# Kernel optimization log

Measured on AMD Instinct MI355X. Metric: run time of the kernel, lower is better.

Reference implementation:

```python
import jax, jax.numpy as jnp
import numpy as np

B, S, D = 1, 4096, 1024
H = 16
HD = D // H  # 64
ROPE_THETA = 10000.0
NEG_INF = -1e9


def setup_inputs() -> dict:
    key = jax.random.key(0)
    ks = jax.random.split(key, 6)
    x = jax.random.normal(ks[0], (B, S, D), dtype=jnp.float32)
    # rotary frequencies: freqs_cis = exp(i * t * theta^{-2j/hd}), j in [0, hd/2)
    inv_freq = 1.0 / (ROPE_THETA ** (jnp.arange(0, HD, 2, dtype=jnp.float32) / HD))  # [HD/2]
    angles = jnp.arange(S, dtype=jnp.float32)[:, None] * inv_freq[None, :]  # [S, HD/2]
    freqs_cos = jnp.cos(angles)
    freqs_sin = jnp.sin(angles)
    # causal additive mask [S, S]
    mask = jnp.where(jnp.triu(jnp.ones((S, S), dtype=bool), k=1), NEG_INF, 0.0).astype(jnp.float32)
    scale = 0.02
    wq = jax.random.normal(ks[1], (D, D), dtype=jnp.float32) * scale
    wk = jax.random.normal(ks[2], (D, D), dtype=jnp.float32) * scale
    wv = jax.random.normal(ks[3], (D, D), dtype=jnp.float32) * scale
    wo = jax.random.normal(ks[4], (D, D), dtype=jnp.float32) * scale
    return {"x": x, "freqs_cos": freqs_cos, "freqs_sin": freqs_sin, "mask": mask,
            "wq": wq, "wk": wk, "wv": wv, "wo": wo}


def _apply_rope(t, cos, sin):
    # t: [B, S, H, HD]; cos/sin: [S, HD/2] -> broadcast [1, S, 1, HD/2]
    tr = t.reshape(*t.shape[:-1], HD // 2, 2)
    te, to = tr[..., 0], tr[..., 1]
    c = cos[None, :, None, :]
    s = sin[None, :, None, :]
    # complex multiply (te + i*to) * (c + i*s)
    oe = te * c - to * s
    oo = te * s + to * c
    return jnp.stack([oe, oo], axis=-1).reshape(t.shape)


def reference(x, freqs_cos, freqs_sin, mask, wq, wk, wv, wo):
    b, s, d = x.shape
    q = (x @ wq.T).reshape(b, s, H, HD)
    k = (x @ wk.T).reshape(b, s, H, HD)
    v = (x @ wv.T).reshape(b, s, H, HD)
    q = _apply_rope(q, freqs_cos, freqs_sin)
    k = _apply_rope(k, freqs_cos, freqs_sin)
    # [B, H, S, HD]
    q = q.transpose(0, 2, 1, 3)
    k = k.transpose(0, 2, 1, 3)
    v = v.transpose(0, 2, 1, 3)
    scores = jnp.einsum('bhqd,bhkd->bhqk', q, k) / jnp.sqrt(jnp.float32(HD))
    scores = scores + mask[None, None, :, :]
    probs = jax.nn.softmax(scores.astype(jnp.float32), axis=-1).astype(q.dtype)
    out = jnp.einsum('bhqk,bhkd->bhqd', probs, v)
    out = out.transpose(0, 2, 1, 3).reshape(b, s, d)
    return out @ wo.T
```

## Files before the change

### kernel.cpp

```cpp
#include <hip/hip_runtime.h>
#include <stdint.h>

typedef _Float16 f16;
typedef _Float16 v2h __attribute__((ext_vector_type(2)));
typedef _Float16 v4h __attribute__((ext_vector_type(4)));
typedef _Float16 v8h __attribute__((ext_vector_type(8)));
typedef float    v4f __attribute__((ext_vector_type(4)));

#define SEQ 4096
#define NH  16
#define DM  1024
#define QSCALE 0.18033688011112042f
#define MBASE 8.0f

__device__ __forceinline__ float exp2_(float x) {
#if __has_builtin(__builtin_amdgcn_exp2f)
  return __builtin_amdgcn_exp2f(x);
#else
  return exp2f(x);
#endif
}

__device__ __forceinline__ void gload_lds16(const void* g, void* l) {
  __builtin_amdgcn_global_load_lds((const __attribute__((address_space(1))) void*)g,
                                   (__attribute__((address_space(3))) void*)l,
                                   16, 0, 0);
}

#define NX 4194304
#define NW 1048576
__global__ void convert_kernel(const float* __restrict__ x,
                               const float* __restrict__ wq, const float* __restrict__ wk,
                               const float* __restrict__ wv, const float* __restrict__ wo,
                               f16* __restrict__ xf, f16* __restrict__ W, f16* __restrict__ Wo) {
  size_t e = ((size_t)blockIdx.x * 256 + threadIdx.x) * 4;
  const float* src; f16* dst;
  if (e < (size_t)NX) { src = x + e; dst = xf + e; }
  else {
    size_t j = e - NX; int wi = (int)(j >> 20); size_t off = j & (NW - 1);
    src = (wi == 0 ? wq : wi == 1 ? wk : wi == 2 ? wv : wo) + off;
    dst = (wi < 3 ? W + (size_t)wi * NW : Wo) + off;
  }
  v4f v = *(const v4f*)src;
  v4h o = { (f16)v.x, (f16)v.y, (f16)v.z, (f16)v.w };
  *(v4h*)dst = o;
}

template <typename OUTT>
__global__ __launch_bounds__(256, 2) void gemm_bt_f16(const f16* __restrict__ A,
                                                      const f16* __restrict__ B,
                                                      OUTT* __restrict__ C,
                                                      int M, int N, int K) {
  __shared__ __align__(16) f16 As[128 * 64];
  __shared__ __align__(16) f16 Bs[128 * 64];
  const int t = threadIdx.x;
  const int w = t >> 6, l = t & 63, quad = l >> 4, l15 = l & 15;
  const int wm = w & 1, wn = w >> 1;
  const int m0 = blockIdx.y * 128, n0 = blockIdx.x * 128;

  v4f acc[4][4];
#pragma unroll
  for (int i = 0; i < 4; ++i)
#pragma unroll
    for (int j = 0; j < 4; ++j) acc[i][j] = v4f{0.f, 0.f, 0.f, 0.f};

  const int nkt = K >> 6;
  for (int kt = 0; kt < nkt; ++kt) {
    __syncthreads();
#pragma unroll
    for (int i = 0; i < 4; ++i) {
      int c = i * 256 + t; int r = c >> 3, cc = c & 7; int sc = cc ^ (r & 7);
      gload_lds16(A + (size_t)(m0 + r) * K + kt * 64 + sc * 8, As + c * 8);
      gload_lds16(B + (size_t)(n0 + r) * K + kt * 64 + sc * 8, Bs + c * 8);
    }
    __syncthreads();
#pragma unroll
    for (int ks = 0; ks < 2; ++ks) {
      v8h af[4], bf[4];
#pragma unroll
      for (int i = 0; i < 4; ++i) {
        int ra = wm * 64 + i * 16 + l15;
        af[i] = *(const v8h*)(As + ra * 64 + (((ks * 4 + quad) ^ (ra & 7)) * 8));
        int rb = wn * 64 + i * 16 + l15;
        bf[i] = *(const v8h*)(Bs + rb * 64 + (((ks * 4 + quad) ^ (rb & 7)) * 8));
      }
#pragma unroll
      for (int i = 0; i < 4; ++i)
#pragma unroll
        for (int j = 0; j < 4; ++j)
          acc[i][j] = __builtin_amdgcn_mfma_f32_16x16x32_f16(af[i], bf[j], acc[i][j], 0, 0, 0);
    }
  }
#pragma unroll
  for (int i = 0; i < 4; ++i) {
    int m = m0 + wm * 64 + i * 16 + quad * 4;
#pragma unroll
    for (int j = 0; j < 4; ++j) {
      int n = n0 + wn * 64 + j * 16 + l15;
#pragma unroll
      for (int rg = 0; rg < 4; ++rg)
        C[(size_t)(m + rg) * N + n] = (OUTT)acc[i][j][rg];
    }
  }
}

__global__ void rope_kernel(const f16* __restrict__ qkv, const float* __restrict__ fc,
                            const float* __restrict__ fs, f16* __restrict__ Qh,
                            f16* __restrict__ Kh) {
  int idx = blockIdx.x * 256 + threadIdx.x;
  int s = idx >> 9, r = idx & 511, h = r >> 5, i = r & 31;
  size_t base = (size_t)s * 3072 + h * 64 + 2 * i;
  float qe = (float)qkv[base], qo = (float)qkv[base + 1];
  float ke = (float)qkv[base + 1024], ko = (float)qkv[base + 1025];
  float c = fc[s * 32 + i], sn = fs[s * 32 + i];
  size_t ob = ((size_t)(h * 4096 + s)) * 64 + 2 * i;
  v2h qo2 = { (f16)((qe * c - qo * sn) * QSCALE), (f16)((qe * sn + qo * c) * QSCALE) };
  v2h ko2 = { (f16)(ke * c - ko * sn), (f16)(ke * sn + ko * c) };
  *(v2h*)(Qh + ob) = qo2;
  *(v2h*)(Kh + ob) = ko2;
}

__global__ void vtrans_kernel(const f16* __restrict__ qkv, f16* __restrict__ Vt) {
  __shared__ __align__(16) f16 T[64][72];
  int h = blockIdx.x >> 6, sb = blockIdx.x & 63;
  int t = threadIdx.x, s0 = sb * 64;
#pragma unroll
  for (int i = 0; i < 2; ++i) {
    int r = i * 32 + (t >> 3), c8 = t & 7;
    *(v8h*)(&T[r][c8 * 8]) = *(const v8h*)(qkv + (size_t)(s0 + r) * 3072 + 2048 + h * 64 + c8 * 8);
  }
  __syncthreads();
#pragma unroll
  for (int i = 0; i < 4; ++i) {
    int idx = i * 256 + t;
    int d = idx >> 4;
    int sq = (idx & 15) * 4;
    int g = sq >> 5;
    int s32 = sq & 31;
    int kap = ((s32 >> 2) & 3) * 8 + (s32 >> 4) * 4;
    v4h o = { T[sq + 0][d], T[sq + 1][d], T[sq + 2][d], T[sq + 3][d] };
    *(v4h*)(Vt + (size_t)(h * 64 + d) * 4096 + s0 + g * 32 + kap) = o;
  }
}

__global__ __launch_bounds__(256, 2) void flash_kernel(const f16* __restrict__ Qh,
                                                       const f16* __restrict__ Kh,
                                                       const f16* __restrict__ Vt,
                                                       f16* __restrict__ attn) {
  __shared__ __align__(16) f16 SM[16384];
  f16* Ks = SM;
  f16* Vs = SM + 8192;
  int u = blockIdx.x >> 4, h = blockIdx.x & 15;
  int qb = (u < 16) ? (31 - u) : (u - 16);
  int t = threadIdx.x, w = t >> 6, l = t & 63, quad = l >> 4, l15 = l & 15;
  int q0w = qb * 128 + w * 32;

  v8h qf[2][2];
#pragma unroll
  for (int qt = 0; qt < 2; ++qt)
#pragma unroll
    for (int ks = 0; ks < 2; ++ks)
      qf[qt][ks] = *(const v8h*)(Qh + ((size_t)(h * 4096 + q0w + qt * 16 + l15)) * 64 + ks * 32 + quad * 8);

  v4f av[2][4];
#pragma unroll
  for (int qt = 0; qt < 2; ++qt)
#pragma unroll
    for (int db = 0; db < 4; ++db) av[qt][db] = v4f{0.f, 0.f, 0.f, 0.f};
  float lrun[2] = { 0.f, 0.f };

  const int kbhi = 2 * qb + 1;
  const int c0 = t, c1 = 256 + t;
  const int r0 = c0 >> 3, sc0 = (c0 & 7) ^ (r0 & 7);
  const int r1 = c1 >> 3, sc1 = (c1 & 7) ^ (r1 & 7);
  const f16* KhB = Kh + (size_t)h * 4096 * 64;
  const f16* VtB = Vt + (size_t)h * 64 * 4096;

  gload_lds16(KhB + (size_t)r0 * 64 + sc0 * 8, Ks + c0 * 8);
  gload_lds16(KhB + (size_t)r1 * 64 + sc1 * 8, Ks + c1 * 8);
  gload_lds16(VtB + (size_t)r0 * 4096 + sc0 * 8, Vs + c0 * 8);
  gload_lds16(VtB + (size_t)r1 * 4096 + sc1 * 8, Vs + c1 * 8);

  for (int kb = 0; kb <= kbhi; ++kb) {
    __syncthreads();
    if (kb < kbhi) {
      int nb = (kb + 1) & 1;
      int koff = (kb + 1) * 64;
      gload_lds16(KhB + (size_t)(koff + r0) * 64 + sc0 * 8, Ks + nb * 4096 + c0 * 8);
      gload_lds16(KhB + (size_t)(koff + r1) * 64 + sc1 * 8, Ks + nb * 4096 + c1 * 8);
      gload_lds16(VtB + (size_t)r0 * 4096 + koff + sc0 * 8, Vs + nb * 4096 + c0 * 8);
      gload_lds16(VtB + (size_t)r1 * 4096 + koff + sc1 * 8, Vs + nb * 4096 + c1 * 8);
    }
    if (kb * 64 > q0w + 31) continue;
    const f16* Kc = Ks + (kb & 1) * 4096;
    const f16* Vc = Vs + (kb & 1) * 4096;

    v8h kf[4][2];
#pragma unroll
    for (int kt = 0; kt < 4; ++kt)
#pragma unroll
      for (int ks = 0; ks < 2; ++ks) {
        int r = kt * 16 + l15;
        kf[kt][ks] = *(const v8h*)(Kc + r * 64 + (((ks * 4 + quad) ^ (r & 7)) * 8));
      }

#pragma unroll
    for (int qt = 0; qt < 2; ++qt) {
      int qtb = q0w + qt * 16;
      if (kb * 64 > qtb + 15) continue;
      v4f st[4];
#pragma unroll
      for (int kt = 0; kt < 4; ++kt) {
        v4f z = v4f{ -MBASE, -MBASE, -MBASE, -MBASE };
        z = __builtin_amdgcn_mfma_f32_16x16x32_f16(kf[kt][0], qf[qt][0], z, 0, 0, 0);
        st[kt] = __builtin_amdgcn_mfma_f32_16x16x32_f16(kf[kt][1], qf[qt][1], z, 0, 0, 0);
      }
      if (kb * 64 + 63 > qtb) {
        int qg = qtb + l15;
#pragma unroll
        for (int kt = 0; kt < 4; ++kt)
#pragma unroll
          for (int jj = 0; jj < 4; ++jj) {
            int kg = kb * 64 + kt * 16 + quad * 4 + jj;
            if (kg > qg) st[kt][jj] = -1e30f;
          }
      }
      v4h pf[4];
      float rs = 0.f;
#pragma unroll
      for (int kt = 0; kt < 4; ++kt)
#pragma unroll
        for (int jj = 0; jj < 4; ++jj) {
          float p = exp2_(st[kt][jj]);
          rs += p;
          pf[kt][jj] = (f16)p;
        }
      lrun[qt] += rs;
      v8h pg[2];
#pragma unroll
      for (int g = 0; g < 2; ++g) {
        pg[g][0] = pf[2 * g][0]; pg[g][1] = pf[2 * g][1];
        pg[g][2] = pf[2 * g][2]; pg[g][3] = pf[2 * g][3];
        pg[g][4] = pf[2 * g + 1][0]; pg[g][5] = pf[2 * g + 1][1];
        pg[g][6] = pf[2 * g + 1][2]; pg[g][7] = pf[2 * g + 1][3];
      }
#pragma unroll
      for (int db = 0; db < 4; ++db) {
        int r = db * 16 + l15;
#pragma unroll
        for (int g = 0; g < 2; ++g) {
          v8h vf = *(const v8h*)(Vc + r * 64 + (((g * 4 + quad) ^ (r & 7)) * 8));
          av[qt][db] = __builtin_amdgcn_mfma_f32_16x16x32_f16(vf, pg[g], av[qt][db], 0, 0, 0);
        }
      }
    }
  }
  __syncthreads();
  f16* Epi = SM + w * 2304;
#pragma unroll
  for (int qt = 0; qt < 2; ++qt) {
    float lr = lrun[qt];
    lr += __shfl_xor(lr, 16);
    lr += __shfl_xor(lr, 32);
    float inv = 1.f / lr;
#pragma unroll
    for (int db = 0; db < 4; ++db)
#pragma unroll
      for (int rg = 0; rg < 4; ++rg)
        Epi[(qt * 16 + l15) * 72 + db * 16 + quad * 4 + rg] = (f16)(av[qt][db][rg] * inv);
  }
  __syncthreads();
  int rr = l >> 1, half = l & 1;
#pragma unroll
  for (int c = 0; c < 4; ++c) {
    v8h v = *(const v8h*)(&Epi[rr * 72 + half * 32 + c * 8]);
    *(v8h*)(attn + (size_t)(q0w + rr) * 1024 + h * 64 + half * 32 + c * 8) = v;
  }
}

extern "C" void kernel_launch(void* const* d_in, const int* in_sizes, int n_in,
                              void* d_out, int out_size, void* d_ws, size_t ws_size,
                              hipStream_t stream) {
  (void)in_sizes; (void)n_in; (void)out_size; (void)ws_size;
  const float* x  = (const float*)d_in[0];
  const float* fc = (const float*)d_in[1];
  const float* fs = (const float*)d_in[2];
  const float* wq = (const float*)d_in[4];
  const float* wk = (const float*)d_in[5];
  const float* wv = (const float*)d_in[6];
  const float* wo = (const float*)d_in[7];
  float* out = (float*)d_out;
  char* ws = (char*)d_ws;

  f16* xf   = (f16*)(ws);
  f16* W    = (f16*)(ws + 8388608);
  f16* Wo   = (f16*)(ws + 14680064);
  f16* QKV  = (f16*)(ws + 16777216);
  f16* Qh   = (f16*)(ws + 41943040);
  f16* Kh   = (f16*)(ws + 50331648);
  f16* Vt   = (f16*)(ws + 58720256);
  f16* attn = xf;

  convert_kernel<<<dim3(8192), dim3(256), 0, stream>>>(x, wq, wk, wv, wo, xf, W, Wo);
  gemm_bt_f16<f16><<<dim3(24, 32), dim3(256), 0, stream>>>(xf, W, QKV, 4096, 3072, 1024);
  rope_kernel<<<dim3(8192), dim3(256), 0, stream>>>(QKV, fc, fs, Qh, Kh);
  vtrans_kernel<<<dim3(1024), dim3(256), 0, stream>>>(QKV, Vt);
  flash_kernel<<<dim3(512), dim3(256), 0, stream>>>(Qh, Kh, Vt, attn);
  gemm_bt_f16<float><<<dim3(8, 32), dim3(256), 0, stream>>>(attn, Wo, out, 4096, 1024, 1024);
}
```

Before: 250.1 us.

## Split causal attention KV range across blocks and add combine kernel

Each query block's causal KV range is split into 1-4 chunks depending on its length, giving 1280 roughly balanced blocks instead of 512 unequal ones. Unnormalized partial outputs and row sums go to workspace, and a new combine kernel sums and normalizes them. Launch bounds are raised to allow more resident blocks. This adds extra global traffic for the partials, one more launch, and possible register pressure from the higher occupancy target.

Measured after the change: 353.8 us. +41.5%, slower.

```diff
diff --git a/kernel.cpp b/kernel.cpp
--- a/kernel.cpp
+++ b/kernel.cpp
@@ -143,17 +143,26 @@
   }
 }
 
-__global__ __launch_bounds__(256, 2) void flash_kernel(const f16* __restrict__ Qh,
+__global__ __launch_bounds__(256, 5) void flash_kernel(const f16* __restrict__ Qh,
                                                        const f16* __restrict__ Kh,
                                                        const f16* __restrict__ Vt,
-                                                       f16* __restrict__ attn) {
+                                                       f16* __restrict__ Opart,
+                                                       float* __restrict__ Lpart) {
   __shared__ __align__(16) f16 SM[16384];
   f16* Ks = SM;
   f16* Vs = SM + 8192;
-  int u = blockIdx.x >> 4, h = blockIdx.x & 15;
-  int qb = (u < 16) ? (31 - u) : (u - 16);
-  int t = threadIdx.x, w = t >> 6, l = t & 63, quad = l >> 4, l15 = l & 15;
-  int q0w = qb * 128 + w * 32;
+  const int h = blockIdx.y;
+  const int sr = 79 - (int)blockIdx.x;
+  int qb, sp, nsp;
+  if (sr < 8)       { qb = sr; sp = 0; nsp = 1; }
+  else if (sr < 24) { int j = sr - 8;  qb = 8  + (j >> 1); sp = j & 1; nsp = 2; }
+  else if (sr < 48) { int j = sr - 24; int q3 = j / 3; qb = 16 + q3; sp = j - 3 * q3; nsp = 3; }
+  else              { int j = sr - 48; qb = 24 + (j >> 2); sp = j & 3; nsp = 4; }
+  const int S = 2 * qb + 2;
+  const int lo = (sp * S) / nsp, hi = ((sp + 1) * S) / nsp - 1;
+
+  const int t = threadIdx.x, w = t >> 6, l = t & 63, quad = l >> 4, l15 = l & 15;
+  const int q0w = qb * 128 + w * 32;
 
   v8h qf[2][2];
 #pragma unroll
@@ -169,21 +178,25 @@
     for (int db = 0; db < 4; ++db) av[qt][db] = v4f{0.f, 0.f, 0.f, 0.f};
   float lrun[2] = { 0.f, 0.f };
 
-  const int kbhi = 2 * qb + 1;
   const int c0 = t, c1 = 256 + t;
   const int r0 = c0 >> 3, sc0 = (c0 & 7) ^ (r0 & 7);
   const int r1 = c1 >> 3, sc1 = (c1 & 7) ^ (r1 & 7);
   const f16* KhB = Kh + (size_t)h * 4096 * 64;
   const f16* VtB = Vt + (size_t)h * 64 * 4096;
 
-  gload_lds16(KhB + (size_t)r0 * 64 + sc0 * 8, Ks + c0 * 8);
-  gload_lds16(KhB + (size_t)r1 * 64 + sc1 * 8, Ks + c1 * 8);
-  gload_lds16(VtB + (size_t)r0 * 4096 + sc0 * 8, Vs + c0 * 8);
-  gload_lds16(VtB + (size_t)r1 * 4096 + sc1 * 8, Vs + c1 * 8);
-
-  for (int kb = 0; kb <= kbhi; ++kb) {
+  {
+    int koff = lo * 64;
+    f16* Kd = Ks + (lo & 1) * 4096;
+    f16* Vd = Vs + (lo & 1) * 4096;
+    gload_lds16(KhB + (size_t)(koff + r0) * 64 + sc0 * 8, Kd + c0 * 8);
+    gload_lds16(KhB + (size_t)(koff + r1) * 64 + sc1 * 8, Kd + c1 * 8);
+    gload_lds16(VtB + (size_t)r0 * 4096 + koff + sc0 * 8, Vd + c0 * 8);
+    gload_lds16(VtB + (size_t)r1 * 4096 + koff + sc1 * 8, Vd + c1 * 8);
+  }
+
+  for (int kb = lo; kb <= hi; ++kb) {
     __syncthreads();
-    if (kb < kbhi) {
+    if (kb < hi) {
       int nb = (kb + 1) & 1;
       int koff = (kb + 1) * 64;
       gload_lds16(KhB + (size_t)(koff + r0) * 64 + sc0 * 8, Ks + nb * 4096 + c0 * 8);
@@ -255,26 +268,54 @@
       }
     }
   }
-  __syncthreads();
-  f16* Epi = SM + w * 2304;
+  const size_t base = (size_t)(h * 80 + sr);
 #pragma unroll
   for (int qt = 0; qt < 2; ++qt) {
     float lr = lrun[qt];
     lr += __shfl_xor(lr, 16);
     lr += __shfl_xor(lr, 32);
-    float inv = 1.f / lr;
-#pragma unroll
-    for (int db = 0; db < 4; ++db)
-#pragma unroll
-      for (int rg = 0; rg < 4; ++rg)
-        Epi[(qt * 16 + l15) * 72 + db * 16 + quad * 4 + rg] = (f16)(av[qt][db][rg] * inv);
-  }
-  __syncthreads();
-  int rr = l >> 1, half = l & 1;
+    int q = w * 32 + qt * 16 + l15;
+    if (quad == 0) Lpart[base * 128 + q] = lr;
+#pragma unroll
+    for (int db = 0; db < 4; ++db) {
+      v4h o = { (f16)av[qt][db][0], (f16)av[qt][db][1],
+                (f16)av[qt][db][2], (f16)av[qt][db][3] };
+      *(v4h*)(Opart + base * 8192 + (size_t)q * 64 + db * 16 + quad * 4) = o;
+    }
+  }
+}
+
+__global__ void combine_kernel(const f16* __restrict__ Opart, const float* __restrict__ Lpart,
+                               f16* __restrict__ attn) {
+  int qb = blockIdx.x, h = blockIdx.y;
+  int nsp, base;
+  if (qb < 8)       { nsp = 1; base = qb; }
+  else if (qb < 16) { nsp = 2; base = 8 + 2 * (qb - 8); }
+  else if (qb < 24) { nsp = 3; base = 24 + 3 * (qb - 16); }
+  else              { nsp = 4; base = 48 + 4 * (qb - 24); }
+  int t = threadIdx.x, q = t >> 1, dh = (t & 1) * 32;
+  float l = 0.f;
+  float o[32];
+#pragma unroll
+  for (int c = 0; c < 32; ++c) o[c] = 0.f;
+  for (int s = 0; s < nsp; ++s) {
+    size_t sb = (size_t)(h * 80 + base + s);
+    const f16* P = Opart + sb * 8192 + q * 64 + dh;
+#pragma unroll
+    for (int c = 0; c < 4; ++c) {
+      v8h v = *(const v8h*)(P + c * 8);
+#pragma unroll
+      for (int j = 0; j < 8; ++j) o[c * 8 + j] += (float)v[j];
+    }
+    l += Lpart[sb * 128 + q];
+  }
+  float inv = 1.f / l;
 #pragma unroll
   for (int c = 0; c < 4; ++c) {
-    v8h v = *(const v8h*)(&Epi[rr * 72 + half * 32 + c * 8]);
-    *(v8h*)(attn + (size_t)(q0w + rr) * 1024 + h * 64 + half * 32 + c * 8) = v;
+    v8h v;
+#pragma unroll
+    for (int j = 0; j < 8; ++j) v[j] = (f16)(o[c * 8 + j] * inv);
+    *(v8h*)(attn + (size_t)(qb * 128 + q) * 1024 + h * 64 + dh + c * 8) = v;
   }
 }
 
@@ -292,19 +333,22 @@
   float* out = (float*)d_out;
   char* ws = (char*)d_ws;
 
-  f16* xf   = (f16*)(ws);
-  f16* W    = (f16*)(ws + 8388608);
-  f16* Wo   = (f16*)(ws + 14680064);
-  f16* QKV  = (f16*)(ws + 16777216);
-  f16* Qh   = (f16*)(ws + 41943040);
-  f16* Kh   = (f16*)(ws + 50331648);
-  f16* Vt   = (f16*)(ws + 58720256);
-  f16* attn = xf;
+  f16* xf    = (f16*)(ws);
+  f16* W     = (f16*)(ws + 8388608);
+  f16* Wo    = (f16*)(ws + 14680064);
+  f16* QKV   = (f16*)(ws + 16777216);
+  f16* Qh    = (f16*)(ws + 41943040);
+  f16* Kh    = (f16*)(ws + 50331648);
+  f16* Vt    = (f16*)(ws + 58720256);
+  f16* attn  = xf;
+  f16* Opart = QKV;
+  float* Lpart = (float*)(ws + 16777216 + 20971520);
 
   convert_kernel<<<dim3(8192), dim3(256), 0, stream>>>(x, wq, wk, wv, wo, xf, W, Wo);
   gemm_bt_f16<f16><<<dim3(24, 32), dim3(256), 0, stream>>>(xf, W, QKV, 4096, 3072, 1024);
   rope_kernel<<<dim3(8192), dim3(256), 0, stream>>>(QKV, fc, fs, Qh, Kh);
   vtrans_kernel<<<dim3(1024), dim3(256), 0, stream>>>(QKV, Vt);
-  flash_kernel<<<dim3(512), dim3(256), 0, stream>>>(Qh, Kh, Vt, attn);
+  flash_kernel<<<dim3(80, 16), dim3(256), 0, stream>>>(Qh, Kh, Vt, Opart, Lpart);
+  combine_kernel<<<dim3(32, 16), dim3(256), 0, stream>>>(Opart, Lpart, attn);
   gemm_bt_f16<float><<<dim3(8, 32), dim3(256), 0, stream>>>(attn, Wo, out, 4096, 1024, 1024);
 }
```
